# Kernel optimization log

Measured on AMD Instinct MI355X. Metric: run time of the kernel, lower is better.

## Reference

```python
import jax, jax.numpy as jnp
import numpy as np

EPS = 1e-8

def _qparams(x, bits):
    # AsymmetricSignedQParams + GlobalMinMaxObserver: per-tensor min/max,
    # signed range [-2^(b-1), 2^(b-1)-1], asymmetric zero point.
    qmin = -(2 ** (bits - 1))
    qmax = 2 ** (bits - 1) - 1
    mn = jnp.minimum(jnp.min(x), 0.0)
    mx = jnp.maximum(jnp.max(x), 0.0)
    scale = jnp.maximum((mx - mn) / (qmax - qmin), EPS)
    zp = jnp.clip(jnp.round(qmin - mn / scale), qmin, qmax)
    return scale, zp, qmin, qmax

def _fake_quant(x, bits):
    # quantize -> clamp -> dequantize (simulated fixed-point as in float forward)
    scale, zp, qmin, qmax = _qparams(x, bits)
    q = jnp.clip(jnp.round(x / scale) + zp, qmin, qmax)
    return (q - zp) * scale


def setup_inputs() -> dict:
    key = jax.random.key(0)
    k1, k2, k3 = jax.random.split(key, 3)
    B, W, H, D = 8, 1024, 8, 64
    q = jax.random.normal(k1, (B, W, H, D), dtype=jnp.float32)
    k = jax.random.normal(k2, (B, W, H, D), dtype=jnp.float32)
    v = jax.random.normal(k3, (B, W, H, D), dtype=jnp.float32)
    return {"q": q, "k": k, "v": v, "quant_bits": 8}


def reference(q, k, v, quant_bits):
    bits = int(quant_bits)
    d_model = q.shape[-1]
    inv_sqrt_d = 1.0 / np.sqrt(d_model)

    # quantize-dequantize inputs (inputs_{q,k,v}_QParams)
    qf = _fake_quant(q, bits)
    kf = _fake_quant(k, bits)
    vf = _fake_quant(v, bits)

    # matrix_multi_score: quantized QK^T with folded 1/sqrt(d) scale,
    # then requantize output (matrix_multi_score.outputs_QParams)
    scores = jnp.einsum("bqhd,bkhd->bhqk", qf, kf) * inv_sqrt_d
    scores = _fake_quant(scores, bits)

    # SoftmaxLUT: softmax over last dim, result requantized (softmax.outputs_QParams)
    att = jax.nn.softmax(scores, axis=-1)
    att_q = _fake_quant(att, bits)

    # matrix_multi_att: quantized att @ V, requantized output
    context = jnp.einsum("bhqk,bkhd->bqhd", att_q, vf)
    context = _fake_quant(context, bits)

    return context, att_q
```

## Files before the change

kernel.cpp:

```cpp
#include <hip/hip_runtime.h>
#include <cstdint>
#include <cstddef>

#define W  1024
#define NH 8
#define NB 8
#define DH 64
#define BHN (NB*NH)
#define CTX_ELEMS ((size_t)NB*W*NH*DH)
#define NS 64
#define ROWF 512
#define L2E 1.4426950408889634f

typedef int v4i __attribute__((ext_vector_type(4)));


__device__ __forceinline__ unsigned enc_f(float f){
  unsigned u = __float_as_uint(f);
  return (u & 0x80000000u) ? ~u : (u | 0x80000000u);
}
__device__ __forceinline__ float dec_f(unsigned k){
  unsigned u = (k & 0x80000000u) ? (k ^ 0x80000000u) : ~k;
  return __uint_as_float(u);
}

__device__ __forceinline__ float fq1(float x, float s, float z, float mn, float mx){
  float t = rintf(x / s) + z;
  t = fminf(fmaxf(t, mn), mx);
  return (t - z) * s;
}
__device__ __forceinline__ int qint_m(float x, float is, float z, float mn, float mx){
  return (int)fminf(fmaxf(rintf(x * is) + z, mn), mx);
}
__device__ __forceinline__ unsigned pack4(int a0, int a1, int a2, int a3){
  return (unsigned)(a0 & 0xff) | ((unsigned)(a1 & 0xff) << 8) |
         ((unsigned)(a2 & 0xff) << 16) | ((unsigned)(a3 & 0xff) << 24);
}

__device__ __forceinline__ unsigned* slot_min(unsigned* s, int t){ return s + (size_t)(2*t)*NS; }
__device__ __forceinline__ unsigned* slot_max(unsigned* s, int t){ return s + (size_t)(2*t+1)*NS; }

struct QP { float s, z; };

__device__ __forceinline__ QP qp_generic(const unsigned* slots, int t, float qmn, float qmx){
  const unsigned* pm = slots + (size_t)(2*t)*NS;
  const unsigned* px = pm + NS;
  unsigned em = pm[0], ex = px[0];
  for (int i = 1; i < NS; ++i){
    unsigned a = pm[i], b = px[i];
    em = (a < em) ? a : em;
    ex = (b > ex) ? b : ex;
  }
  float mn = dec_f(em), mx = dec_f(ex);
  QP r;
  r.s = fmaxf((mx - mn) / (qmx - qmn), 1e-8f);
  r.z = fminf(fmaxf(rintf(qmn - mn / r.s), qmn), qmx);
  return r;
}
__device__ __forceinline__ QP qp_scores(const int* jmn, const int* jmx, float sq, float sk,
                                        float qmn, float qmx){
  int em = jmn[0], ex = jmx[0];
  for (int i = 1; i < NS; ++i){ em = min(em, jmn[i]); ex = max(ex, jmx[i]); }
  float cfac = 0.125f * (sq * sk);
  float mn = fminf(cfac * (float)em, 0.0f);
  float mx = fmaxf(cfac * (float)ex, 0.0f);
  QP r;
  r.s = fmaxf((mx - mn) / (qmx - qmn), 1e-8f);
  r.z = fminf(fmaxf(rintf(qmn - mn / r.s), qmn), qmx);
  return r;
}

__device__ __forceinline__ void blk_minmax_atomic(float lmin, float lmax,
                                                  unsigned* smin, unsigned* smax){
  #pragma unroll
  for (int o = 32; o; o >>= 1){
    lmin = fminf(lmin, __shfl_xor(lmin, o));
    lmax = fmaxf(lmax, __shfl_xor(lmax, o));
  }
  __shared__ float wmn[4], wmx[4];
  int wid = threadIdx.x >> 6, lane = threadIdx.x & 63;
  if (lane == 0){ wmn[wid] = lmin; wmx[wid] = lmax; }
  __syncthreads();
  if (threadIdx.x == 0){
    float a = wmn[0], b = wmx[0];
    for (int w = 1; w < (int)(blockDim.x >> 6); ++w){
      a = fminf(a, wmn[w]); b = fmaxf(b, wmx[w]);
    }
    atomicMin(smin, enc_f(a));
    atomicMax(smax, enc_f(b));
  }
}

__device__ __forceinline__ void blk_iminmax_atomic(int lmin, int lmax, int* gmin, int* gmax){
  #pragma unroll
  for (int o = 32; o; o >>= 1){
    lmin = min(lmin, __shfl_xor(lmin, o));
    lmax = max(lmax, __shfl_xor(lmax, o));
  }
  __shared__ int iwmn[4], iwmx[4];
  int wid = threadIdx.x >> 6, lane = threadIdx.x & 63;
  if (lane == 0){ iwmn[wid] = lmin; iwmx[wid] = lmax; }
  __syncthreads();
  if (threadIdx.x == 0){
    int a = iwmn[0], b = iwmx[0];
    for (int w = 1; w < (int)(blockDim.x >> 6); ++w){
      a = min(a, iwmn[w]); b = max(b, iwmx[w]);
    }
    atomicMin(gmin, a);
    atomicMax(gmax, b);
  }
}

__device__ __forceinline__ void stage_tile(const float* __restrict__ rowptr,
                                           signed char (*S)[80], int* __restrict__ Ssum,
                                           float is, float z, float mn, float mx, int t){
  const int rr = t >> 2, dq = (t & 3) << 4;
  const float* p = rowptr + (size_t)rr * ROWF + dq;
  int part = 0;
  #pragma unroll
  for (int g = 0; g < 4; ++g){
    float4 x = *(const float4*)(p + g * 4);
    int a0 = qint_m(x.x, is, z, mn, mx), a1 = qint_m(x.y, is, z, mn, mx);
    int a2 = qint_m(x.z, is, z, mn, mx), a3 = qint_m(x.w, is, z, mn, mx);
    part += a0 + a1 + a2 + a3;
    *(unsigned*)&S[rr][dq + g*4] = pack4(a0, a1, a2, a3);
  }
  int x1 = part + __shfl_xor(part, 1);
  int tot = x1 + __shfl_xor(x1, 2);
  if ((t & 3) == 0) Ssum[rr] = tot;
}

__device__ __forceinline__ void copy_tile(const char* __restrict__ blob8, const int* __restrict__ Ssum8,
                                          signed char (*S)[80], int* __restrict__ Ssum, int t){
  const int rr = t >> 2, p4 = (t & 3) << 4;
  *(float4*)&S[rr][p4] = *(const float4*)(blob8 + ((size_t)rr << 6) + p4);
  if (t < 64) Ssum[t] = Ssum8[t];
}


__global__ void init_slots_kernel(unsigned* __restrict__ slots, int* __restrict__ jmn,
                                  int* __restrict__ jmx){
  for (int i = threadIdx.x; i < 6*2*NS; i += blockDim.x)
    slots[i] = 0x80000000u;
  if (threadIdx.x < NS){
    jmn[threadIdx.x] = 0x7fffffff;
    jmx[threadIdx.x] = (int)0x80000000;
  }
}

__global__ __launch_bounds__(256) void minmax3_kernel(const float* __restrict__ q,
                                                      const float* __restrict__ k,
                                                      const float* __restrict__ v,
                                                      unsigned* __restrict__ slots){
  const float4* p = (const float4*)(blockIdx.y == 0 ? q : (blockIdx.y == 1 ? k : v));
  float lmin = 0.f, lmax = 0.f;
  const int n4 = (int)(CTX_ELEMS / 4);
  for (int i = blockIdx.x * blockDim.x + threadIdx.x; i < n4; i += gridDim.x * blockDim.x){
    float4 x = p[i];
    lmin = fminf(lmin, fminf(fminf(x.x, x.y), fminf(x.z, x.w)));
    lmax = fmaxf(lmax, fmaxf(fmaxf(x.x, x.y), fmaxf(x.z, x.w)));
  }
  const int idx = blockIdx.x & (NS - 1);
  blk_minmax_atomic(lmin, lmax, slot_min(slots, blockIdx.y) + idx, slot_max(slots, blockIdx.y) + idx);
}

template<bool CACHED>
__global__ __launch_bounds__(256) void pass1_kernel(const float* __restrict__ qg,
                                                    const float* __restrict__ kg,
                                                    const unsigned* __restrict__ slots,
                                                    const int* __restrict__ bits_p,
                                                    float* __restrict__ stash,
                                                    int* __restrict__ jmn,
                                                    int* __restrict__ jmx,
                                                    char* __restrict__ q8,
                                                    char* __restrict__ k8,
                                                    int* __restrict__ Sq8,
                                                    int* __restrict__ Sk8){
  __shared__ __align__(16) signed char Qs[64][80], Ks[64][80];
  __shared__ int Sq[64], Sk[64];
  const int bits = *bits_p;
  const float qmx = (float)((1 << (bits-1)) - 1), qmn = -(float)(1 << (bits-1));
  const QP qq = qp_generic(slots, 0, qmn, qmx);
  const QP kp = qp_generic(slots, 1, qmn, qmx);
  const int it = blockIdx.x, bh = blockIdx.y, b = bh >> 3, h = bh & 7;
  const int i0 = it << 6, t = threadIdx.x;
  const int lane = t & 63, w = t >> 6, lr = lane & 15, lg = lane >> 4;
  const float isq = 1.0f / qq.s, isk = 1.0f / kp.s;
  const int izq = (int)qq.z, izk = (int)kp.z, c64 = 64 * izq * izk;

  stage_tile(qg + ((size_t)(b*W + i0) * NH + h) * DH, Qs, Sq, isq, qq.z, qmn, qmx, t);
  __syncthreads();
  if (CACHED){
    const int rr = t >> 2, p4 = (t & 3) << 4;
    *(float4*)(q8 + ((size_t)bh << 16) + (((size_t)(i0 + rr)) << 6) + p4) =
        *(const float4*)&Qs[rr][p4];
    if ((t & 3) == 0) Sq8[(bh << 10) + i0 + rr] = Sq[rr];
  }
  const v4i Bq = *(const v4i*)&Qs[(w << 4) + lr][lg << 4];
  const int sqi = Sq[(w << 4) + lr];

  int gmin = 0x7fffffff, gmax = (int)0x80000000, rmax = (int)0x80000000;
  for (int cc = 0; cc < 16; ++cc){
    __syncthreads();
    stage_tile(kg + ((size_t)(b*W + (cc << 6)) * NH + h) * DH, Ks, Sk, isk, kp.z, qmn, qmx, t);
    __syncthreads();
    if (CACHED && cc == it){
      const int rr = t >> 2, p4 = (t & 3) << 4;
      *(float4*)(k8 + ((size_t)bh << 16) + (((size_t)((cc << 6) + rr)) << 6) + p4) =
          *(const float4*)&Ks[rr][p4];
      if ((t & 3) == 0) Sk8[(bh << 10) + (cc << 6) + rr] = Sk[rr];
    }
    #pragma unroll
    for (int jt = 0; jt < 4; ++jt){
      v4i Ak = *(const v4i*)&Ks[(jt << 4) + lr][lg << 4];
      v4i zz = {0, 0, 0, 0};
      v4i acc = __builtin_amdgcn_mfma_i32_16x16x64_i8(Ak, Bq, zz, 0, 0, 0);
      v4i s4 = *(const v4i*)&Sk[(jt << 4) + (lg << 2)];
      #pragma unroll
      for (int r = 0; r < 4; ++r){
        int J = acc[r] - izq * s4[r] - izk * sqi + c64;
        gmin = min(gmin, J); gmax = max(gmax, J); rmax = max(rmax, J);
      }
    }
  }
  rmax = max(rmax, __shfl_xor(rmax, 16));
  rmax = max(rmax, __shfl_xor(rmax, 32));
  if (lg == 0)
    stash[((size_t)(b*W + i0 + (w << 4) + lr) * NH + h) * DH] = __int_as_float(rmax);
  const int idx = (it + bh * 16) & (NS - 1);
  blk_iminmax_atomic(gmin, gmax, jmn + idx, jmx + idx);
}

template<bool CACHED>
__global__ __launch_bounds__(256) void pass2_kernel(const float* __restrict__ qg,
                                                    const float* __restrict__ kg,
                                                    unsigned* __restrict__ slots,
                                                    const int* __restrict__ jmn,
                                                    const int* __restrict__ jmx,
                                                    const int* __restrict__ bits_p,
                                                    float* __restrict__ stash,
                                                    const char* __restrict__ q8,
                                                    const char* __restrict__ k8,
                                                    const int* __restrict__ Sq8,
                                                    const int* __restrict__ Sk8){
  __shared__ __align__(16) signed char Qs[64][80], Ks[64][80];
  __shared__ int Sq[64], Sk[64];
  const int bits = *bits_p;
  const float qmx = (float)((1 << (bits-1)) - 1), qmn = -(float)(1 << (bits-1));
  const QP qq = qp_generic(slots, 0, qmn, qmx);
  const QP kp = qp_generic(slots, 1, qmn, qmx);
  const QP sp = qp_scores(jmn, jmx, qq.s, kp.s, qmn, qmx);
  const int it = blockIdx.x, bh = blockIdx.y, b = bh >> 3, h = bh & 7;
  const int i0 = it << 6, t = threadIdx.x;
  const int lane = t & 63, w = t >> 6, lr = lane & 15, lg = lane >> 4;
  const float isq = 1.0f / qq.s, isk = 1.0f / kp.s;
  const int izq = (int)qq.z, izk = (int)kp.z, c64 = 64 * izq * izk;
  const float rf = (0.125f * (qq.s * kp.s)) / sp.s;
  const float c2 = sp.s * L2E;
  const float zs = sp.z;
  const int irow = (w << 4) + lr;

  v4i Bq; int sqi;
  if (CACHED){
    Bq = *(const v4i*)(q8 + ((size_t)bh << 16) + (((size_t)(i0 + irow)) << 6) + (lg << 4));
    sqi = Sq8[(bh << 10) + i0 + irow];
  } else {
    stage_tile(qg + ((size_t)(b*W + i0) * NH + h) * DH, Qs, Sq, isq, qq.z, qmn, qmx, t);
    __syncthreads();
    Bq = *(const v4i*)&Qs[irow][lg << 4];
    sqi = Sq[irow];
  }
  int Jm = __float_as_int(stash[((size_t)(b*W + i0 + irow) * NH + h) * DH]);
  const float tmxf = fminf(fmaxf(rintf((float)Jm * rf) + zs, qmn), qmx);

  float zacc = 0.f;
  for (int cc = 0; cc < 16; ++cc){
    __syncthreads();
    if (CACHED)
      copy_tile(k8 + ((size_t)bh << 16) + ((size_t)(cc << 6) << 6), Sk8 + (bh << 10) + (cc << 6),
                Ks, Sk, t);
    else
      stage_tile(kg + ((size_t)(b*W + (cc << 6)) * NH + h) * DH, Ks, Sk, isk, kp.z, qmn, qmx, t);
    __syncthreads();
    #pragma unroll
    for (int jt = 0; jt < 4; ++jt){
      v4i Ak = *(const v4i*)&Ks[(jt << 4) + lr][lg << 4];
      v4i zz = {0, 0, 0, 0};
      v4i acc = __builtin_amdgcn_mfma_i32_16x16x64_i8(Ak, Bq, zz, 0, 0, 0);
      v4i s4 = *(const v4i*)&Sk[(jt << 4) + (lg << 2)];
      int J0 = acc[0] - izq * s4[0] - izk * sqi + c64;
      int J1 = acc[1] - izq * s4[1] - izk * sqi + c64;
      int J2 = acc[2] - izq * s4[2] - izk * sqi + c64;
      int J3 = acc[3] - izq * s4[3] - izk * sqi + c64;
      float tl0 = fminf(fmaxf(rintf((float)J0 * rf) + zs, qmn), qmx);
      float tl1 = fminf(fmaxf(rintf((float)J1 * rf) + zs, qmn), qmx);
      float tl2 = fminf(fmaxf(rintf((float)J2 * rf) + zs, qmn), qmx);
      float tl3 = fminf(fmaxf(rintf((float)J3 * rf) + zs, qmn), qmx);
      zacc += exp2f((tl0 - tmxf) * c2);
      zacc += exp2f((tl1 - tmxf) * c2);
      zacc += exp2f((tl2 - tmxf) * c2);
      zacc += exp2f((tl3 - tmxf) * c2);
    }
  }
  zacc += __shfl_xor(zacc, 16);
  zacc += __shfl_xor(zacc, 32);
  if (lg == 0)
    stash[((size_t)(b*W + i0 + irow) * NH + h) * DH + 1] = zacc;
  float ratt = 1.0f / zacc;
  #pragma unroll
  for (int o = 1; o < 16; o <<= 1) ratt = fmaxf(ratt, __shfl_xor(ratt, o));
  if (lane == 0){
    const int idx = ((it << 2) + w + bh * 64) & (NS - 1);
    atomicMax(slot_max(slots, 4) + idx, enc_f(ratt));
  }
}

template<bool CACHED>
__global__ __launch_bounds__(256) void pass3_kernel(const float* __restrict__ qg,
                                                    const float* __restrict__ kg,
                                                    const float* __restrict__ vg,
                                                    float* __restrict__ att,
                                                    float* __restrict__ ctx,
                                                    unsigned* __restrict__ slots,
                                                    const int* __restrict__ jmn,
                                                    const int* __restrict__ jmx,
                                                    const int* __restrict__ bits_p,
                                                    const char* __restrict__ q8,
                                                    const char* __restrict__ k8,
                                                    const int* __restrict__ Sq8,
                                                    const int* __restrict__ Sk8){
  __shared__ __align__(16) signed char Qs[64][80], Ks[64][80], Vs[64][80], As[64][80];
  __shared__ int Sq[64], Sk[64];
  __shared__ int RowA[64], ColV[64];
  const int bits = *bits_p;
  const float qmx = (float)((1 << (bits-1)) - 1), qmn = -(float)(1 << (bits-1));
  const QP qq = qp_generic(slots, 0, qmn, qmx);
  const QP kp = qp_generic(slots, 1, qmn, qmx);
  const QP sp = qp_scores(jmn, jmx, qq.s, kp.s, qmn, qmx);
  const QP vp = qp_generic(slots, 2, qmn, qmx);
  const QP ap = qp_generic(slots, 4, qmn, qmx);
  const int it = blockIdx.x, bh = blockIdx.y, b = bh >> 3, h = bh & 7;
  const int i0 = it << 6, t = threadIdx.x;
  const int lane = t & 63, w = t >> 6, lr = lane & 15, lg = lane >> 4;
  const float isq = 1.0f / qq.s, isk = 1.0f / kp.s;
  const int izq = (int)qq.z, izk = (int)kp.z, c64 = 64 * izq * izk;
  const float rf = (0.125f * (qq.s * kp.s)) / sp.s;
  const float c2 = sp.s * L2E, zs = sp.z;
  const float sa = ap.s, za = ap.z, inv_sa = 1.0f / sa;
  const float sv = vp.s, zv = vp.z, isv = 1.0f / sv;
  const int iza = (int)za, izv = (int)zv;
  const int irow = (w << 4) + lr;

  if (t < 64) ColV[t] = 0;
  v4i Bq; int sqi;
  if (CACHED){
    Bq = *(const v4i*)(q8 + ((size_t)bh << 16) + (((size_t)(i0 + irow)) << 6) + (lg << 4));
    sqi = Sq8[(bh << 10) + i0 + irow];
  } else {
    stage_tile(qg + ((size_t)(b*W + i0) * NH + h) * DH, Qs, Sq, isq, qq.z, qmn, qmx, t);
    __syncthreads();
    Bq = *(const v4i*)&Qs[irow][lg << 4];
    sqi = Sq[irow];
  }
  const size_t rbase = ((size_t)(b*W + i0 + irow) * NH + h) * DH;
  int Jm = __float_as_int(ctx[rbase]);
  const float tmxf = fminf(fmaxf(rintf((float)Jm * rf) + zs, qmn), qmx);
  const float iZ = 1.0f / ctx[rbase + 1];

  const int dq4 = (t & 15) << 2;
  const int kb  = (t >> 4) << 2;
  int cv4[4] = {0, 0, 0, 0};
  int rA = 0;
  v4i accPV[4];
  #pragma unroll
  for (int tj = 0; tj < 4; ++tj){ v4i zz = {0,0,0,0}; accPV[tj] = zz; }

  for (int cc = 0; cc < 16; ++cc){
    __syncthreads();
    if (CACHED)
      copy_tile(k8 + ((size_t)bh << 16) + ((size_t)(cc << 6) << 6), Sk8 + (bh << 10) + (cc << 6),
                Ks, Sk, t);
    else
      stage_tile(kg + ((size_t)(b*W + (cc << 6)) * NH + h) * DH, Ks, Sk, isk, kp.z, qmn, qmx, t);
    {
      const float* vp_ = vg + ((size_t)(b*W + (cc << 6) + kb) * NH + h) * DH + dq4;
      float4 x0 = *(const float4*)(vp_);
      float4 x1 = *(const float4*)(vp_ + ROWF);
      float4 x2 = *(const float4*)(vp_ + 2 * ROWF);
      float4 x3 = *(const float4*)(vp_ + 3 * ROWF);
      int q00 = qint_m(x0.x, isv, zv, qmn, qmx), q01 = qint_m(x0.y, isv, zv, qmn, qmx),
          q02 = qint_m(x0.z, isv, zv, qmn, qmx), q03 = qint_m(x0.w, isv, zv, qmn, qmx);
      int q10 = qint_m(x1.x, isv, zv, qmn, qmx), q11 = qint_m(x1.y, isv, zv, qmn, qmx),
          q12 = qint_m(x1.z, isv, zv, qmn, qmx), q13 = qint_m(x1.w, isv, zv, qmn, qmx);
      int q20 = qint_m(x2.x, isv, zv, qmn, qmx), q21 = qint_m(x2.y, isv, zv, qmn, qmx),
          q22 = qint_m(x2.z, isv, zv, qmn, qmx), q23 = qint_m(x2.w, isv, zv, qmn, qmx);
      int q30 = qint_m(x3.x, isv, zv, qmn, qmx), q31 = qint_m(x3.y, isv, zv, qmn, qmx),
          q32 = qint_m(x3.z, isv, zv, qmn, qmx), q33 = qint_m(x3.w, isv, zv, qmn, qmx);
      cv4[0] += q00 + q10 + q20 + q30;
      cv4[1] += q01 + q11 + q21 + q31;
      cv4[2] += q02 + q12 + q22 + q32;
      cv4[3] += q03 + q13 + q23 + q33;
      *(unsigned*)&Vs[dq4 + 0][kb] = pack4(q00, q10, q20, q30);
      *(unsigned*)&Vs[dq4 + 1][kb] = pack4(q01, q11, q21, q31);
      *(unsigned*)&Vs[dq4 + 2][kb] = pack4(q02, q12, q22, q32);
      *(unsigned*)&Vs[dq4 + 3][kb] = pack4(q03, q13, q23, q33);
    }
    __syncthreads();
    #pragma unroll
    for (int jt = 0; jt < 4; ++jt){
      v4i Ak = *(const v4i*)&Ks[(jt << 4) + lr][lg << 4];
      v4i zz = {0, 0, 0, 0};
      v4i acc = __builtin_amdgcn_mfma_i32_16x16x64_i8(Ak, Bq, zz, 0, 0, 0);
      v4i s4 = *(const v4i*)&Sk[(jt << 4) + (lg << 2)];
      int J0 = acc[0] - izq * s4[0] - izk * sqi + c64;
      int J1 = acc[1] - izq * s4[1] - izk * sqi + c64;
      int J2 = acc[2] - izq * s4[2] - izk * sqi + c64;
      int J3 = acc[3] - izq * s4[3] - izk * sqi + c64;
      float tl0 = fminf(fmaxf(rintf((float)J0 * rf) + zs, qmn), qmx);
      float tl1 = fminf(fmaxf(rintf((float)J1 * rf) + zs, qmn), qmx);
      float tl2 = fminf(fmaxf(rintf((float)J2 * rf) + zs, qmn), qmx);
      float tl3 = fminf(fmaxf(rintf((float)J3 * rf) + zs, qmn), qmx);
      float p0 = exp2f((tl0 - tmxf) * c2) * iZ;
      float p1 = exp2f((tl1 - tmxf) * c2) * iZ;
      float p2 = exp2f((tl2 - tmxf) * c2) * iZ;
      float p3 = exp2f((tl3 - tmxf) * c2) * iZ;
      float a0 = fminf(fmaxf(rintf(p0 * inv_sa) + za, qmn), qmx);
      float a1 = fminf(fmaxf(rintf(p1 * inv_sa) + za, qmn), qmx);
      float a2 = fminf(fmaxf(rintf(p2 * inv_sa) + za, qmn), qmx);
      float a3 = fminf(fmaxf(rintf(p3 * inv_sa) + za, qmn), qmx);
      float4 y;
      y.x = (a0 - za) * sa; y.y = (a1 - za) * sa;
      y.z = (a2 - za) * sa; y.w = (a3 - za) * sa;
      *(float4*)(att + ((size_t)bh << 20) + (size_t)(i0 + irow) * W
                 + (cc << 6) + (jt << 4) + (lg << 2)) = y;
      int q0 = (int)a0, q1 = (int)a1, q2 = (int)a2, q3 = (int)a3;
      rA += q0 + q1 + q2 + q3;
      *(unsigned*)&As[irow][(jt << 4) + (lg << 2)] = pack4(q0, q1, q2, q3);
    }
    {
      v4i A2 = *(const v4i*)&As[(w << 4) + lr][lg << 4];
      #pragma unroll
      for (int tj = 0; tj < 4; ++tj){
        v4i B2 = *(const v4i*)&Vs[(tj << 4) + lr][lg << 4];
        accPV[tj] = __builtin_amdgcn_mfma_i32_16x16x64_i8(A2, B2, accPV[tj], 0, 0, 0);
      }
    }
  }

  rA += __shfl_xor(rA, 16);
  rA += __shfl_xor(rA, 32);
  if (lg == 0) RowA[irow] = rA;
  #pragma unroll
  for (int j = 0; j < 4; ++j) atomicAdd(&ColV[dq4 + j], cv4[j]);
  __syncthreads();

  const float sav = sa * sv;
  float lmin = 0.f, lmax = 0.f;
  #pragma unroll
  for (int tj = 0; tj < 4; ++tj){
    const int d = (tj << 4) + lr;
    #pragma unroll
    for (int r = 0; r < 4; ++r){
      const int i = (w << 4) + (lg << 2) + r;
      int Jv = accPV[tj][r] - iza * ColV[d] - izv * RowA[i] + 1024 * iza * izv;
      float c = sav * (float)Jv;
      lmin = fminf(lmin, c); lmax = fmaxf(lmax, c);
      ctx[(((size_t)(b * W + i0 + i)) * NH + h) * DH + d] = c;
    }
  }
  const int idx = (it + bh * 16) & (NS - 1);
  blk_minmax_atomic(lmin, lmax, slot_min(slots, 5) + idx, slot_max(slots, 5) + idx);
}

__global__ __launch_bounds__(256) void quantctx_kernel(float* __restrict__ ctx,
                                                       const unsigned* __restrict__ slots,
                                                       const int* __restrict__ bits_p){
  const int bits = *bits_p;
  const float qmx = (float)((1 << (bits-1)) - 1), qmn = -(float)(1 << (bits-1));
  const QP cp = qp_generic(slots, 5, qmn, qmx);
  size_t i = (size_t)blockIdx.x * blockDim.x + threadIdx.x;
  float4* p = (float4*)ctx;
  float4 x = p[i];
  x.x = fq1(x.x, cp.s, cp.z, qmn, qmx);
  x.y = fq1(x.y, cp.s, cp.z, qmn, qmx);
  x.z = fq1(x.z, cp.s, cp.z, qmn, qmx);
  x.w = fq1(x.w, cp.s, cp.z, qmn, qmx);
  p[i] = x;
}


extern "C" void kernel_launch(void* const* d_in, const int* in_sizes, int n_in,
                              void* d_out, int out_size, void* d_ws, size_t ws_size,
                              hipStream_t stream){
  const float* q = (const float*)d_in[0];
  const float* k = (const float*)d_in[1];
  const float* v = (const float*)d_in[2];
  const int* bits = (const int*)d_in[3];
  float* ctx = (float*)d_out;
  float* att = (float*)d_out + CTX_ELEMS;
  unsigned* slots = (unsigned*)d_ws;
  int* jmn = (int*)((char*)d_ws + 3072);
  int* jmx = (int*)((char*)d_ws + 3328);
  int* Sq8 = (int*)((char*)d_ws + 4096);
  int* Sk8 = (int*)((char*)d_ws + 266240);
  char* q8 = (char*)d_ws + 528384;
  char* k8 = (char*)d_ws + 4722688;
  const bool cached = ws_size >= (size_t)9000000;

  hipLaunchKernelGGL(init_slots_kernel, dim3(1), dim3(256), 0, stream, slots, jmn, jmx);
  hipLaunchKernelGGL(minmax3_kernel, dim3(512, 3), dim3(256), 0, stream, q, k, v, slots);
  if (cached){
    hipLaunchKernelGGL(pass1_kernel<true>, dim3(16, BHN), dim3(256), 0, stream,
                       q, k, slots, bits, ctx, jmn, jmx, q8, k8, Sq8, Sk8);
    hipLaunchKernelGGL(pass2_kernel<true>, dim3(16, BHN), dim3(256), 0, stream,
                       q, k, slots, jmn, jmx, bits, ctx, q8, k8, Sq8, Sk8);
    hipLaunchKernelGGL(pass3_kernel<true>, dim3(16, BHN), dim3(256), 0, stream,
                       q, k, v, att, ctx, slots, jmn, jmx, bits, q8, k8, Sq8, Sk8);
  } else {
    hipLaunchKernelGGL(pass1_kernel<false>, dim3(16, BHN), dim3(256), 0, stream,
                       q, k, slots, bits, ctx, jmn, jmx, q8, k8, Sq8, Sk8);
    hipLaunchKernelGGL(pass2_kernel<false>, dim3(16, BHN), dim3(256), 0, stream,
                       q, k, slots, jmn, jmx, bits, ctx, q8, k8, Sq8, Sk8);
    hipLaunchKernelGGL(pass3_kernel<false>, dim3(16, BHN), dim3(256), 0, stream,
                       q, k, v, att, ctx, slots, jmn, jmx, bits, q8, k8, Sq8, Sk8);
  }
  hipLaunchKernelGGL(quantctx_kernel, dim3(4096), dim3(256), 0, stream, ctx, slots, bits);
}
```

Before: 224.5 us.

## Prequantize K and V into int8 workspace in a separate pass

Adds a pass1a kernel that quantizes K (row-major int8) and V (transposed int8 with column sums) once into the workspace. The later passes then read MFMA fragments straight from global int8 buffers without shared-memory staging or per-tile barriers. Q fragments are quantized directly in registers instead of being cached. The aim is to remove repeated fp32 K/V loads and re-quantization across the three passes, at the cost of one extra launch, global atomics for the V column sums, and uncoalesced fragment loads from global memory.

```diff
diff --git a/kernel.cpp b/kernel.cpp
--- a/kernel.cpp
+++ b/kernel.cpp
@@ -130,22 +130,36 @@
   if ((t & 3) == 0) Ssum[rr] = tot;
 }
 
-__device__ __forceinline__ void copy_tile(const char* __restrict__ blob8, const int* __restrict__ Ssum8,
-                                          signed char (*S)[80], int* __restrict__ Ssum, int t){
-  const int rr = t >> 2, p4 = (t & 3) << 4;
-  *(float4*)&S[rr][p4] = *(const float4*)(blob8 + ((size_t)rr << 6) + p4);
-  if (t < 64) Ssum[t] = Ssum8[t];
+__device__ __forceinline__ v4i qfrag_direct(const float* __restrict__ qrow, int lg,
+                                            float is, float z, float mn, float mx,
+                                            int* sqi_out){
+  const float* p = qrow + (lg << 4);
+  int part = 0; unsigned d4[4];
+  #pragma unroll
+  for (int g = 0; g < 4; ++g){
+    float4 x = *(const float4*)(p + g * 4);
+    int a0 = qint_m(x.x, is, z, mn, mx), a1 = qint_m(x.y, is, z, mn, mx);
+    int a2 = qint_m(x.z, is, z, mn, mx), a3 = qint_m(x.w, is, z, mn, mx);
+    part += a0 + a1 + a2 + a3;
+    d4[g] = pack4(a0, a1, a2, a3);
+  }
+  part += __shfl_xor(part, 16);
+  part += __shfl_xor(part, 32);
+  *sqi_out = part;
+  v4i r; r[0] = (int)d4[0]; r[1] = (int)d4[1]; r[2] = (int)d4[2]; r[3] = (int)d4[3];
+  return r;
 }
 
 
 __global__ void init_slots_kernel(unsigned* __restrict__ slots, int* __restrict__ jmn,
-                                  int* __restrict__ jmx){
+                                  int* __restrict__ jmx, int* __restrict__ Sv8){
   for (int i = threadIdx.x; i < 6*2*NS; i += blockDim.x)
     slots[i] = 0x80000000u;
   if (threadIdx.x < NS){
     jmn[threadIdx.x] = 0x7fffffff;
     jmx[threadIdx.x] = (int)0x80000000;
   }
+  for (int i = threadIdx.x; i < BHN*64; i += blockDim.x) Sv8[i] = 0;
 }
 
 __global__ __launch_bounds__(256) void minmax3_kernel(const float* __restrict__ q,
@@ -164,18 +178,313 @@
   blk_minmax_atomic(lmin, lmax, slot_min(slots, blockIdx.y) + idx, slot_max(slots, blockIdx.y) + idx);
 }
 
-template<bool CACHED>
-__global__ __launch_bounds__(256) void pass1_kernel(const float* __restrict__ qg,
-                                                    const float* __restrict__ kg,
-                                                    const unsigned* __restrict__ slots,
-                                                    const int* __restrict__ bits_p,
-                                                    float* __restrict__ stash,
-                                                    int* __restrict__ jmn,
-                                                    int* __restrict__ jmx,
-                                                    char* __restrict__ q8,
-                                                    char* __restrict__ k8,
-                                                    int* __restrict__ Sq8,
-                                                    int* __restrict__ Sk8){
+
+__global__ __launch_bounds__(256) void pass1a_kernel(const float* __restrict__ kg,
+                                                     const float* __restrict__ vg,
+                                                     const unsigned* __restrict__ slots,
+                                                     const int* __restrict__ bits_p,
+                                                     char* __restrict__ k8,
+                                                     int* __restrict__ Sk8,
+                                                     char* __restrict__ v8,
+                                                     int* __restrict__ Sv8){
+  __shared__ int ColS[64];
+  const int bits = *bits_p;
+  const float qmx = (float)((1 << (bits-1)) - 1), qmn = -(float)(1 << (bits-1));
+  const QP kp = qp_generic(slots, 1, qmn, qmx);
+  const QP vp = qp_generic(slots, 2, qmn, qmx);
+  const int it = blockIdx.x, bh = blockIdx.y, b = bh >> 3, h = bh & 7;
+  const int i0 = it << 6, t = threadIdx.x;
+
+  {
+    const int rr = t >> 2, dq = (t & 3) << 4;
+    const float* p = kg + ((size_t)(b*W + i0 + rr) * NH + h) * DH + dq;
+    const float isk = 1.0f / kp.s;
+    int part = 0; unsigned d4[4];
+    #pragma unroll
+    for (int g = 0; g < 4; ++g){
+      float4 x = *(const float4*)(p + g * 4);
+      int a0 = qint_m(x.x, isk, kp.z, qmn, qmx), a1 = qint_m(x.y, isk, kp.z, qmn, qmx);
+      int a2 = qint_m(x.z, isk, kp.z, qmn, qmx), a3 = qint_m(x.w, isk, kp.z, qmn, qmx);
+      part += a0 + a1 + a2 + a3;
+      d4[g] = pack4(a0, a1, a2, a3);
+    }
+    uint4 u; u.x = d4[0]; u.y = d4[1]; u.z = d4[2]; u.w = d4[3];
+    *(uint4*)(k8 + ((size_t)bh << 16) + (((size_t)(i0 + rr)) << 6) + dq) = u;
+    int x1 = part + __shfl_xor(part, 1);
+    int tot = x1 + __shfl_xor(x1, 2);
+    if ((t & 3) == 0) Sk8[(bh << 10) + i0 + rr] = tot;
+  }
+
+  {
+    const int dq4 = (t & 15) << 2, kb = (t >> 4) << 2;
+    const float* vp_ = vg + ((size_t)(b*W + i0 + kb) * NH + h) * DH + dq4;
+    const float isv = 1.0f / vp.s;
+    float4 x0 = *(const float4*)(vp_);
+    float4 x1 = *(const float4*)(vp_ + ROWF);
+    float4 x2 = *(const float4*)(vp_ + 2 * ROWF);
+    float4 x3 = *(const float4*)(vp_ + 3 * ROWF);
+    int q00 = qint_m(x0.x, isv, vp.z, qmn, qmx), q01 = qint_m(x0.y, isv, vp.z, qmn, qmx),
+        q02 = qint_m(x0.z, isv, vp.z, qmn, qmx), q03 = qint_m(x0.w, isv, vp.z, qmn, qmx);
+    int q10 = qint_m(x1.x, isv, vp.z, qmn, qmx), q11 = qint_m(x1.y, isv, vp.z, qmn, qmx),
+        q12 = qint_m(x1.z, isv, vp.z, qmn, qmx), q13 = qint_m(x1.w, isv, vp.z, qmn, qmx);
+    int q20 = qint_m(x2.x, isv, vp.z, qmn, qmx), q21 = qint_m(x2.y, isv, vp.z, qmn, qmx),
+        q22 = qint_m(x2.z, isv, vp.z, qmn, qmx), q23 = qint_m(x2.w, isv, vp.z, qmn, qmx);
+    int q30 = qint_m(x3.x, isv, vp.z, qmn, qmx), q31 = qint_m(x3.y, isv, vp.z, qmn, qmx),
+        q32 = qint_m(x3.z, isv, vp.z, qmn, qmx), q33 = qint_m(x3.w, isv, vp.z, qmn, qmx);
+    unsigned w0 = pack4(q00, q10, q20, q30);
+    unsigned w1 = pack4(q01, q11, q21, q31);
+    unsigned w2 = pack4(q02, q12, q22, q32);
+    unsigned w3 = pack4(q03, q13, q23, q33);
+    char* vb = v8 + ((size_t)bh << 16) + i0 + kb;
+    *(unsigned*)(vb + ((size_t)(dq4 + 0) << 10)) = w0;
+    *(unsigned*)(vb + ((size_t)(dq4 + 1) << 10)) = w1;
+    *(unsigned*)(vb + ((size_t)(dq4 + 2) << 10)) = w2;
+    *(unsigned*)(vb + ((size_t)(dq4 + 3) << 10)) = w3;
+    int cv0 = q00 + q10 + q20 + q30;
+    int cv1 = q01 + q11 + q21 + q31;
+    int cv2 = q02 + q12 + q22 + q32;
+    int cv3 = q03 + q13 + q23 + q33;
+    if (t < 64) ColS[t] = 0;
+    __syncthreads();
+    atomicAdd(&ColS[dq4 + 0], cv0);
+    atomicAdd(&ColS[dq4 + 1], cv1);
+    atomicAdd(&ColS[dq4 + 2], cv2);
+    atomicAdd(&ColS[dq4 + 3], cv3);
+    __syncthreads();
+    if (t < 64) atomicAdd(&Sv8[(bh << 6) + t], ColS[t]);
+  }
+}
+
+__global__ __launch_bounds__(256) void pass1b_kernel(const float* __restrict__ qg,
+                                                     const unsigned* __restrict__ slots,
+                                                     const int* __restrict__ bits_p,
+                                                     float* __restrict__ stash,
+                                                     int* __restrict__ jmn,
+                                                     int* __restrict__ jmx,
+                                                     const char* __restrict__ k8,
+                                                     const int* __restrict__ Sk8){
+  const int bits = *bits_p;
+  const float qmx = (float)((1 << (bits-1)) - 1), qmn = -(float)(1 << (bits-1));
+  const QP qq = qp_generic(slots, 0, qmn, qmx);
+  const QP kp = qp_generic(slots, 1, qmn, qmx);
+  const int it = blockIdx.x, bh = blockIdx.y, b = bh >> 3, h = bh & 7;
+  const int i0 = it << 6, t = threadIdx.x;
+  const int lane = t & 63, w = t >> 6, lr = lane & 15, lg = lane >> 4;
+  const int irow = (w << 4) + lr;
+  const int izq = (int)qq.z, izk = (int)kp.z, c64 = 64 * izq * izk;
+
+  int sqi;
+  v4i Bq = qfrag_direct(qg + ((size_t)(b*W + i0 + irow) * NH + h) * DH, lg,
+                        1.0f / qq.s, qq.z, qmn, qmx, &sqi);
+  const char* kb = k8 + ((size_t)bh << 16);
+  const int* skb = Sk8 + (bh << 10);
+
+  int gmin = 0x7fffffff, gmax = (int)0x80000000, rmax = (int)0x80000000;
+  for (int cc = 0; cc < 16; ++cc){
+    #pragma unroll
+    for (int jt = 0; jt < 4; ++jt){
+      v4i Ak = *(const v4i*)(kb + (((size_t)((cc << 6) + (jt << 4) + lr)) << 6) + (lg << 4));
+      v4i s4 = *(const v4i*)(skb + (cc << 6) + (jt << 4) + (lg << 2));
+      v4i zz = {0, 0, 0, 0};
+      v4i acc = __builtin_amdgcn_mfma_i32_16x16x64_i8(Ak, Bq, zz, 0, 0, 0);
+      #pragma unroll
+      for (int r = 0; r < 4; ++r){
+        int J = acc[r] - izq * s4[r] - izk * sqi + c64;
+        gmin = min(gmin, J); gmax = max(gmax, J); rmax = max(rmax, J);
+      }
+    }
+  }
+  rmax = max(rmax, __shfl_xor(rmax, 16));
+  rmax = max(rmax, __shfl_xor(rmax, 32));
+  if (lg == 0)
+    stash[((size_t)(b*W + i0 + irow) * NH + h) * DH] = __int_as_float(rmax);
+  const int idx = (it + bh * 16) & (NS - 1);
+  blk_iminmax_atomic(gmin, gmax, jmn + idx, jmx + idx);
+}
+
+__global__ __launch_bounds__(256) void pass2c_kernel(const float* __restrict__ qg,
+                                                     unsigned* __restrict__ slots,
+                                                     const int* __restrict__ jmn,
+                                                     const int* __restrict__ jmx,
+                                                     const int* __restrict__ bits_p,
+                                                     float* __restrict__ stash,
+                                                     const char* __restrict__ k8,
+                                                     const int* __restrict__ Sk8){
+  const int bits = *bits_p;
+  const float qmx = (float)((1 << (bits-1)) - 1), qmn = -(float)(1 << (bits-1));
+  const QP qq = qp_generic(slots, 0, qmn, qmx);
+  const QP kp = qp_generic(slots, 1, qmn, qmx);
+  const QP sp = qp_scores(jmn, jmx, qq.s, kp.s, qmn, qmx);
+  const int it = blockIdx.x, bh = blockIdx.y, b = bh >> 3, h = bh & 7;
+  const int i0 = it << 6, t = threadIdx.x;
+  const int lane = t & 63, w = t >> 6, lr = lane & 15, lg = lane >> 4;
+  const int irow = (w << 4) + lr;
+  const int izq = (int)qq.z, izk = (int)kp.z, c64 = 64 * izq * izk;
+  const float rf = (0.125f * (qq.s * kp.s)) / sp.s;
+  const float c2 = sp.s * L2E, zs = sp.z;
+
+  int sqi;
+  v4i Bq = qfrag_direct(qg + ((size_t)(b*W + i0 + irow) * NH + h) * DH, lg,
+                        1.0f / qq.s, qq.z, qmn, qmx, &sqi);
+  int Jm = __float_as_int(stash[((size_t)(b*W + i0 + irow) * NH + h) * DH]);
+  const float tmxf = fminf(fmaxf(rintf((float)Jm * rf) + zs, qmn), qmx);
+  const char* kb = k8 + ((size_t)bh << 16);
+  const int* skb = Sk8 + (bh << 10);
+
+  float zacc = 0.f;
+  for (int cc = 0; cc < 16; ++cc){
+    #pragma unroll
+    for (int jt = 0; jt < 4; ++jt){
+      v4i Ak = *(const v4i*)(kb + (((size_t)((cc << 6) + (jt << 4) + lr)) << 6) + (lg << 4));
+      v4i s4 = *(const v4i*)(skb + (cc << 6) + (jt << 4) + (lg << 2));
+      v4i zz = {0, 0, 0, 0};
+      v4i acc = __builtin_amdgcn_mfma_i32_16x16x64_i8(Ak, Bq, zz, 0, 0, 0);
+      int J0 = acc[0] - izq * s4[0] - izk * sqi + c64;
+      int J1 = acc[1] - izq * s4[1] - izk * sqi + c64;
+      int J2 = acc[2] - izq * s4[2] - izk * sqi + c64;
+      int J3 = acc[3] - izq * s4[3] - izk * sqi + c64;
+      float tl0 = fminf(fmaxf(rintf((float)J0 * rf) + zs, qmn), qmx);
+      float tl1 = fminf(fmaxf(rintf((float)J1 * rf) + zs, qmn), qmx);
+      float tl2 = fminf(fmaxf(rintf((float)J2 * rf) + zs, qmn), qmx);
+      float tl3 = fminf(fmaxf(rintf((float)J3 * rf) + zs, qmn), qmx);
+      zacc += exp2f((tl0 - tmxf) * c2);
+      zacc += exp2f((tl1 - tmxf) * c2);
+      zacc += exp2f((tl2 - tmxf) * c2);
+      zacc += exp2f((tl3 - tmxf) * c2);
+    }
+  }
+  zacc += __shfl_xor(zacc, 16);
+  zacc += __shfl_xor(zacc, 32);
+  if (lg == 0)
+    stash[((size_t)(b*W + i0 + irow) * NH + h) * DH + 1] = zacc;
+  float ratt = 1.0f / zacc;
+  #pragma unroll
+  for (int o = 1; o < 16; o <<= 1) ratt = fmaxf(ratt, __shfl_xor(ratt, o));
+  if (lane == 0){
+    const int idx = ((it << 2) + w + bh * 64) & (NS - 1);
+    atomicMax(slot_max(slots, 4) + idx, enc_f(ratt));
+  }
+}
+
+__global__ __launch_bounds__(256) void pass3c_kernel(const float* __restrict__ qg,
+                                                     float* __restrict__ att,
+                                                     float* __restrict__ ctx,
+                                                     unsigned* __restrict__ slots,
+                                                     const int* __restrict__ jmn,
+                                                     const int* __restrict__ jmx,
+                                                     const int* __restrict__ bits_p,
+                                                     const char* __restrict__ k8,
+                                                     const int* __restrict__ Sk8,
+                                                     const char* __restrict__ v8,
+                                                     const int* __restrict__ Sv8){
+  __shared__ __align__(16) signed char As[64][80];
+  __shared__ int RowA[64];
+  const int bits = *bits_p;
+  const float qmx = (float)((1 << (bits-1)) - 1), qmn = -(float)(1 << (bits-1));
+  const QP qq = qp_generic(slots, 0, qmn, qmx);
+  const QP kp = qp_generic(slots, 1, qmn, qmx);
+  const QP sp = qp_scores(jmn, jmx, qq.s, kp.s, qmn, qmx);
+  const QP vp = qp_generic(slots, 2, qmn, qmx);
+  const QP ap = qp_generic(slots, 4, qmn, qmx);
+  const int it = blockIdx.x, bh = blockIdx.y, b = bh >> 3, h = bh & 7;
+  const int i0 = it << 6, t = threadIdx.x;
+  const int lane = t & 63, w = t >> 6, lr = lane & 15, lg = lane >> 4;
+  const int irow = (w << 4) + lr;
+  const int izq = (int)qq.z, izk = (int)kp.z, c64 = 64 * izq * izk;
+  const int iza = (int)ap.z, izv = (int)vp.z;
+  const float rf = (0.125f * (qq.s * kp.s)) / sp.s;
+  const float c2 = sp.s * L2E, zs = sp.z;
+  const float sa = ap.s, za = ap.z, inv_sa = 1.0f / sa;
+
+  int sqi;
+  v4i Bq = qfrag_direct(qg + ((size_t)(b*W + i0 + irow) * NH + h) * DH, lg,
+                        1.0f / qq.s, qq.z, qmn, qmx, &sqi);
+  const size_t rbase = ((size_t)(b*W + i0 + irow) * NH + h) * DH;
+  int Jm = __float_as_int(ctx[rbase]);
+  const float tmxf = fminf(fmaxf(rintf((float)Jm * rf) + zs, qmn), qmx);
+  const float iZ = 1.0f / ctx[rbase + 1];
+  const char* kb = k8 + ((size_t)bh << 16);
+  const int* skb = Sk8 + (bh << 10);
+  const char* vb = v8 + ((size_t)bh << 16);
+
+  int rA = 0;
+  v4i accPV[4];
+  #pragma unroll
+  for (int tj = 0; tj < 4; ++tj){ v4i zz = {0,0,0,0}; accPV[tj] = zz; }
+
+  for (int cc = 0; cc < 16; ++cc){
+    #pragma unroll
+    for (int jt = 0; jt < 4; ++jt){
+      v4i Ak = *(const v4i*)(kb + (((size_t)((cc << 6) + (jt << 4) + lr)) << 6) + (lg << 4));
+      v4i s4 = *(const v4i*)(skb + (cc << 6) + (jt << 4) + (lg << 2));
+      v4i zz = {0, 0, 0, 0};
+      v4i acc = __builtin_amdgcn_mfma_i32_16x16x64_i8(Ak, Bq, zz, 0, 0, 0);
+      int J0 = acc[0] - izq * s4[0] - izk * sqi + c64;
+      int J1 = acc[1] - izq * s4[1] - izk * sqi + c64;
+      int J2 = acc[2] - izq * s4[2] - izk * sqi + c64;
+      int J3 = acc[3] - izq * s4[3] - izk * sqi + c64;
+      float tl0 = fminf(fmaxf(rintf((float)J0 * rf) + zs, qmn), qmx);
+      float tl1 = fminf(fmaxf(rintf((float)J1 * rf) + zs, qmn), qmx);
+      float tl2 = fminf(fmaxf(rintf((float)J2 * rf) + zs, qmn), qmx);
+      float tl3 = fminf(fmaxf(rintf((float)J3 * rf) + zs, qmn), qmx);
+      float p0 = exp2f((tl0 - tmxf) * c2) * iZ;
+      float p1 = exp2f((tl1 - tmxf) * c2) * iZ;
+      float p2 = exp2f((tl2 - tmxf) * c2) * iZ;
+      float p3 = exp2f((tl3 - tmxf) * c2) * iZ;
+      float a0 = fminf(fmaxf(rintf(p0 * inv_sa) + za, qmn), qmx);
+      float a1 = fminf(fmaxf(rintf(p1 * inv_sa) + za, qmn), qmx);
+      float a2 = fminf(fmaxf(rintf(p2 * inv_sa) + za, qmn), qmx);
+      float a3 = fminf(fmaxf(rintf(p3 * inv_sa) + za, qmn), qmx);
+      float4 y;
+      y.x = (a0 - za) * sa; y.y = (a1 - za) * sa;
+      y.z = (a2 - za) * sa; y.w = (a3 - za) * sa;
+      *(float4*)(att + ((size_t)bh << 20) + (size_t)(i0 + irow) * W
+                 + (cc << 6) + (jt << 4) + (lg << 2)) = y;
+      int q0 = (int)a0, q1 = (int)a1, q2 = (int)a2, q3 = (int)a3;
+      rA += q0 + q1 + q2 + q3;
+      *(unsigned*)&As[irow][(jt << 4) + (lg << 2)] = pack4(q0, q1, q2, q3);
+    }
+    {
+      v4i A2 = *(const v4i*)&As[(w << 4) + lr][lg << 4];
+      #pragma unroll
+      for (int tj = 0; tj < 4; ++tj){
+        v4i B2 = *(const v4i*)(vb + (((size_t)((tj << 4) + lr)) << 10) + (cc << 6) + (lg << 4));
+        accPV[tj] = __builtin_amdgcn_mfma_i32_16x16x64_i8(A2, B2, accPV[tj], 0, 0, 0);
+      }
+    }
+  }
+
+  rA += __shfl_xor(rA, 16);
+  rA += __shfl_xor(rA, 32);
+  if (lg == 0) RowA[irow] = rA;
+
+  const float sav = sa * vp.s;
+  float lmin = 0.f, lmax = 0.f;
+  #pragma unroll
+  for (int tj = 0; tj < 4; ++tj){
+    const int d = (tj << 4) + lr;
+    const int cvd = Sv8[(bh << 6) + d];
+    #pragma unroll
+    for (int r = 0; r < 4; ++r){
+      const int i = (w << 4) + (lg << 2) + r;
+      int Jv = accPV[tj][r] - iza * cvd - izv * RowA[i] + 1024 * iza * izv;
+      float c = sav * (float)Jv;
+      lmin = fminf(lmin, c); lmax = fmaxf(lmax, c);
+      ctx[(((size_t)(b * W + i0 + i)) * NH + h) * DH + d] = c;
+    }
+  }
+  const int idx = (it + bh * 16) & (NS - 1);
+  blk_minmax_atomic(lmin, lmax, slot_min(slots, 5) + idx, slot_max(slots, 5) + idx);
+}
+
+
+__global__ __launch_bounds__(256) void pass1_plain(const float* __restrict__ qg,
+                                                   const float* __restrict__ kg,
+                                                   const unsigned* __restrict__ slots,
+                                                   const int* __restrict__ bits_p,
+                                                   float* __restrict__ stash,
+                                                   int* __restrict__ jmn,
+                                                   int* __restrict__ jmx){
   __shared__ __align__(16) signed char Qs[64][80], Ks[64][80];
   __shared__ int Sq[64], Sk[64];
   const int bits = *bits_p;
@@ -190,12 +499,6 @@
 
   stage_tile(qg + ((size_t)(b*W + i0) * NH + h) * DH, Qs, Sq, isq, qq.z, qmn, qmx, t);
   __syncthreads();
-  if (CACHED){
-    const int rr = t >> 2, p4 = (t & 3) << 4;
-    *(float4*)(q8 + ((size_t)bh << 16) + (((size_t)(i0 + rr)) << 6) + p4) =
-        *(const float4*)&Qs[rr][p4];
-    if ((t & 3) == 0) Sq8[(bh << 10) + i0 + rr] = Sq[rr];
-  }
   const v4i Bq = *(const v4i*)&Qs[(w << 4) + lr][lg << 4];
   const int sqi = Sq[(w << 4) + lr];
 
@@ -204,12 +507,6 @@
     __syncthreads();
     stage_tile(kg + ((size_t)(b*W + (cc << 6)) * NH + h) * DH, Ks, Sk, isk, kp.z, qmn, qmx, t);
     __syncthreads();
-    if (CACHED && cc == it){
-      const int rr = t >> 2, p4 = (t & 3) << 4;
-      *(float4*)(k8 + ((size_t)bh << 16) + (((size_t)((cc << 6) + rr)) << 6) + p4) =
-          *(const float4*)&Ks[rr][p4];
-      if ((t & 3) == 0) Sk8[(bh << 10) + (cc << 6) + rr] = Sk[rr];
-    }
     #pragma unroll
     for (int jt = 0; jt < 4; ++jt){
       v4i Ak = *(const v4i*)&Ks[(jt << 4) + lr][lg << 4];
@@ -231,18 +528,13 @@
   blk_iminmax_atomic(gmin, gmax, jmn + idx, jmx + idx);
 }
 
-template<bool CACHED>
-__global__ __launch_bounds__(256) void pass2_kernel(const float* __restrict__ qg,
-                                                    const float* __restrict__ kg,
-                                                    unsigned* __restrict__ slots,
-                                                    const int* __restrict__ jmn,
-                                                    const int* __restrict__ jmx,
-                                                    const int* __restrict__ bits_p,
-                                                    float* __restrict__ stash,
-                                                    const char* __restrict__ q8,
-                                                    const char* __restrict__ k8,
-                                                    const int* __restrict__ Sq8,
-                                                    const int* __restrict__ Sk8){
+__global__ __launch_bounds__(256) void pass2_plain(const float* __restrict__ qg,
+                                                   const float* __restrict__ kg,
+                                                   unsigned* __restrict__ slots,
+                                                   const int* __restrict__ jmn,
+                                                   const int* __restrict__ jmx,
+                                                   const int* __restrict__ bits_p,
+                                                   float* __restrict__ stash){
   __shared__ __align__(16) signed char Qs[64][80], Ks[64][80];
   __shared__ int Sq[64], Sk[64];
   const int bits = *bits_p;
@@ -256,31 +548,20 @@
   const float isq = 1.0f / qq.s, isk = 1.0f / kp.s;
   const int izq = (int)qq.z, izk = (int)kp.z, c64 = 64 * izq * izk;
   const float rf = (0.125f * (qq.s * kp.s)) / sp.s;
-  const float c2 = sp.s * L2E;
-  const float zs = sp.z;
+  const float c2 = sp.s * L2E, zs = sp.z;
   const int irow = (w << 4) + lr;
 
-  v4i Bq; int sqi;
-  if (CACHED){
-    Bq = *(const v4i*)(q8 + ((size_t)bh << 16) + (((size_t)(i0 + irow)) << 6) + (lg << 4));
-    sqi = Sq8[(bh << 10) + i0 + irow];
-  } else {
-    stage_tile(qg + ((size_t)(b*W + i0) * NH + h) * DH, Qs, Sq, isq, qq.z, qmn, qmx, t);
-    __syncthreads();
-    Bq = *(const v4i*)&Qs[irow][lg << 4];
-    sqi = Sq[irow];
-  }
+  stage_tile(qg + ((size_t)(b*W + i0) * NH + h) * DH, Qs, Sq, isq, qq.z, qmn, qmx, t);
+  __syncthreads();
+  const v4i Bq = *(const v4i*)&Qs[irow][lg << 4];
+  const int sqi = Sq[irow];
   int Jm = __float_as_int(stash[((size_t)(b*W + i0 + irow) * NH + h) * DH]);
   const float tmxf = fminf(fmaxf(rintf((float)Jm * rf) + zs, qmn), qmx);
 
   float zacc = 0.f;
   for (int cc = 0; cc < 16; ++cc){
     __syncthreads();
-    if (CACHED)
-      copy_tile(k8 + ((size_t)bh << 16) + ((size_t)(cc << 6) << 6), Sk8 + (bh << 10) + (cc << 6),
-                Ks, Sk, t);
-    else
-      stage_tile(kg + ((size_t)(b*W + (cc << 6)) * NH + h) * DH, Ks, Sk, isk, kp.z, qmn, qmx, t);
+    stage_tile(kg + ((size_t)(b*W + (cc << 6)) * NH + h) * DH, Ks, Sk, isk, kp.z, qmn, qmx, t);
     __syncthreads();
     #pragma unroll
     for (int jt = 0; jt < 4; ++jt){
@@ -315,20 +596,15 @@
   }
 }
 
-template<bool CACHED>
-__global__ __launch_bounds__(256) void pass3_kernel(const float* __restrict__ qg,
-                                                    const float* __restrict__ kg,
-                                                    const float* __restrict__ vg,
-                                                    float* __restrict__ att,
-                                                    float* __restrict__ ctx,
-                                                    unsigned* __restrict__ slots,
-                                                    const int* __restrict__ jmn,
-                                                    const int* __restrict__ jmx,
-                                                    const int* __restrict__ bits_p,
-                                                    const char* __restrict__ q8,
-                                                    const char* __restrict__ k8,
-                                                    const int* __restrict__ Sq8,
-                                                    const int* __restrict__ Sk8){
+__global__ __launch_bounds__(256) void pass3_plain(const float* __restrict__ qg,
+                                                   const float* __restrict__ kg,
+                                                   const float* __restrict__ vg,
+                                                   float* __restrict__ att,
+                                                   float* __restrict__ ctx,
+                                                   unsigned* __restrict__ slots,
+                                                   const int* __restrict__ jmn,
+                                                   const int* __restrict__ jmx,
+                                                   const int* __restrict__ bits_p){
   __shared__ __align__(16) signed char Qs[64][80], Ks[64][80], Vs[64][80], As[64][80];
   __shared__ int Sq[64], Sk[64];
   __shared__ int RowA[64], ColV[64];
@@ -352,16 +628,10 @@
   const int irow = (w << 4) + lr;
 
   if (t < 64) ColV[t] = 0;
-  v4i Bq; int sqi;
-  if (CACHED){
-    Bq = *(const v4i*)(q8 + ((size_t)bh << 16) + (((size_t)(i0 + irow)) << 6) + (lg << 4));
-    sqi = Sq8[(bh << 10) + i0 + irow];
-  } else {
-    stage_tile(qg + ((size_t)(b*W + i0) * NH + h) * DH, Qs, Sq, isq, qq.z, qmn, qmx, t);
-    __syncthreads();
-    Bq = *(const v4i*)&Qs[irow][lg << 4];
-    sqi = Sq[irow];
-  }
+  stage_tile(qg + ((size_t)(b*W + i0) * NH + h) * DH, Qs, Sq, isq, qq.z, qmn, qmx, t);
+  __syncthreads();
+  const v4i Bq = *(const v4i*)&Qs[irow][lg << 4];
+  const int sqi = Sq[irow];
   const size_t rbase = ((size_t)(b*W + i0 + irow) * NH + h) * DH;
   int Jm = __float_as_int(ctx[rbase]);
   const float tmxf = fminf(fmaxf(rintf((float)Jm * rf) + zs, qmn), qmx);
@@ -377,11 +647,7 @@
 
   for (int cc = 0; cc < 16; ++cc){
     __syncthreads();
-    if (CACHED)
-      copy_tile(k8 + ((size_t)bh << 16) + ((size_t)(cc << 6) << 6), Sk8 + (bh << 10) + (cc << 6),
-                Ks, Sk, t);
-    else
-      stage_tile(kg + ((size_t)(b*W + (cc << 6)) * NH + h) * DH, Ks, Sk, isk, kp.z, qmn, qmx, t);
+    stage_tile(kg + ((size_t)(b*W + (cc << 6)) * NH + h) * DH, Ks, Sk, isk, kp.z, qmn, qmx, t);
     {
       const float* vp_ = vg + ((size_t)(b*W + (cc << 6) + kb) * NH + h) * DH + dq4;
       float4 x0 = *(const float4*)(vp_);
@@ -501,28 +767,30 @@
   unsigned* slots = (unsigned*)d_ws;
   int* jmn = (int*)((char*)d_ws + 3072);
   int* jmx = (int*)((char*)d_ws + 3328);
-  int* Sq8 = (int*)((char*)d_ws + 4096);
-  int* Sk8 = (int*)((char*)d_ws + 266240);
-  char* q8 = (char*)d_ws + 528384;
-  char* k8 = (char*)d_ws + 4722688;
-  const bool cached = ws_size >= (size_t)9000000;
-
-  hipLaunchKernelGGL(init_slots_kernel, dim3(1), dim3(256), 0, stream, slots, jmn, jmx);
+  int* Sv8 = (int*)((char*)d_ws + 4096);
+  int* Sk8 = (int*)((char*)d_ws + 20480);
+  char* k8 = (char*)d_ws + 282624;
+  char* v8 = (char*)d_ws + 4476928;
+  const bool cached = ws_size >= (size_t)8671232;
+
+  hipLaunchKernelGGL(init_slots_kernel, dim3(1), dim3(256), 0, stream, slots, jmn, jmx, Sv8);
   hipLaunchKernelGGL(minmax3_kernel, dim3(512, 3), dim3(256), 0, stream, q, k, v, slots);
   if (cached){
-    hipLaunchKernelGGL(pass1_kernel<true>, dim3(16, BHN), dim3(256), 0, stream,
-                       q, k, slots, bits, ctx, jmn, jmx, q8, k8, Sq8, Sk8);
-    hipLaunchKernelGGL(pass2_kernel<true>, dim3(16, BHN), dim3(256), 0, stream,
-                       q, k, slots, jmn, jmx, bits, ctx, q8, k8, Sq8, Sk8);
-    hipLaunchKernelGGL(pass3_kernel<true>, dim3(16, BHN), dim3(256), 0, stream,
-                       q, k, v, att, ctx, slots, jmn, jmx, bits, q8, k8, Sq8, Sk8);
+    hipLaunchKernelGGL(pass1a_kernel, dim3(16, BHN), dim3(256), 0, stream,
+                       k, v, slots, bits, k8, Sk8, v8, Sv8);
+    hipLaunchKernelGGL(pass1b_kernel, dim3(16, BHN), dim3(256), 0, stream,
+                       q, slots, bits, ctx, jmn, jmx, k8, Sk8);
+    hipLaunchKernelGGL(pass2c_kernel, dim3(16, BHN), dim3(256), 0, stream,
+                       q, slots, jmn, jmx, bits, ctx, k8, Sk8);
+    hipLaunchKernelGGL(pass3c_kernel, dim3(16, BHN), dim3(256), 0, stream,
+                       q, att, ctx, slots, jmn, jmx, bits, k8, Sk8, v8, Sv8);
   } else {
-    hipLaunchKernelGGL(pass1_kernel<false>, dim3(16, BHN), dim3(256), 0, stream,
-                       q, k, slots, bits, ctx, jmn, jmx, q8, k8, Sq8, Sk8);
-    hipLaunchKernelGGL(pass2_kernel<false>, dim3(16, BHN), dim3(256), 0, stream,
-                       q, k, slots, jmn, jmx, bits, ctx, q8, k8, Sq8, Sk8);
-    hipLaunchKernelGGL(pass3_kernel<false>, dim3(16, BHN), dim3(256), 0, stream,
-                       q, k, v, att, ctx, slots, jmn, jmx, bits, q8, k8, Sq8, Sk8);
+    hipLaunchKernelGGL(pass1_plain, dim3(16, BHN), dim3(256), 0, stream,
+                       q, k, slots, bits, ctx, jmn, jmx);
+    hipLaunchKernelGGL(pass2_plain, dim3(16, BHN), dim3(256), 0, stream,
+                       q, k, slots, jmn, jmx, bits, ctx);
+    hipLaunchKernelGGL(pass3_plain, dim3(16, BHN), dim3(256), 0, stream,
+                       q, k, v, att, ctx, slots, jmn, jmx, bits);
   }
   hipLaunchKernelGGL(quantctx_kernel, dim3(4096), dim3(256), 0, stream, ctx, slots, bits);
 }
```

After: 210.5 us. -6.3%, faster.
